# Optimization experiments

Measured on AMD Instinct MI355X. Metric: run time of the kernel, lower is better.

## Reference

```python
import jax, jax.numpy as jnp
import numpy as np

B, DIM, H, W = 8, 512, 32, 32
NUM_HEADS, KEY_DIM, VALUE_DIM, DIM_OUT = 8, 64, 64, 512


def setup_inputs() -> dict:
    key = jax.random.key(0)
    ks = jax.random.split(key, 5)
    return {
        "x": jax.random.normal(ks[0], (B, DIM, H, W), dtype=jnp.float32),
        "query_proj": jax.random.normal(ks[1], (NUM_HEADS, KEY_DIM, DIM), dtype=jnp.float32),
        "key_proj": jax.random.normal(ks[2], (DIM, KEY_DIM), dtype=jnp.float32),
        "value_proj": jax.random.normal(ks[3], (DIM, VALUE_DIM), dtype=jnp.float32),
        "out_proj": jax.random.normal(ks[4], (DIM_OUT, NUM_HEADS, VALUE_DIM), dtype=jnp.float32),
    }


def reference(x, query_proj, key_proj, value_proj, out_proj):
    b, d, h, w = x.shape
    key_dim = query_proj.shape[1]
    scale = key_dim ** (-0.5)
    # flatten spatial dims to tokens: [b, n, d] where n = h*w (m == x here)
    rx = jnp.transpose(x.reshape(b, d, h * w), (0, 2, 1))
    q = jnp.einsum('bnd,hkd->bnhk', rx, query_proj)
    k = jnp.einsum('bmd,dk->bmk', rx, key_proj)          # single shared K head
    attn = jax.nn.softmax(jnp.einsum('bnhk,bmk->bnhm', q, k) * scale, axis=-1)
    v = jnp.einsum('bmd,dv->bmv', rx, value_proj)        # single shared V head
    o = jnp.einsum('bnhm,bmv->bnhv', attn, v)
    result = jnp.einsum('bnhv,dhv->bdn', o, out_proj)
    return result.reshape(b, -1, h, w)
```

## Files before the change

### kernel.cpp

```cpp
#include <hip/hip_runtime.h>
#include <math.h>

#define BATCH 8
#define DIMD  512
#define NTOK  1024
#define NH    8
#define CQKV  640
#define DOUT  512

typedef __attribute__((ext_vector_type(8))) short short8;
typedef __attribute__((ext_vector_type(4))) short short4v;
typedef __attribute__((ext_vector_type(4))) float f32x4;

__device__ __forceinline__ short bf16rn(float x) {
    unsigned u = __float_as_uint(x);
    u += 0x7FFF + ((u >> 16) & 1);
    return (short)(u >> 16);
}
__device__ __forceinline__ float bf16tof(short s) {
    return __uint_as_float(((unsigned)(unsigned short)s) << 16);
}
struct HL { short h, l; };
__device__ __forceinline__ HL bf16split(float x) {
    HL r;
    r.h = bf16rn(x);
    r.l = bf16rn(x - bf16tof(r.h));
    return r;
}
__device__ __forceinline__ void dma16(const short* g, short* l) {
    __builtin_amdgcn_global_load_lds(
        (const __attribute__((address_space(1))) unsigned int*)g,
        (__attribute__((address_space(3))) unsigned int*)l, 16, 0, 0);
}
__device__ __forceinline__ float swzmax16(float v) {
    v = fmaxf(v, __int_as_float(__builtin_amdgcn_ds_swizzle(__float_as_int(v), 0x041F)));
    v = fmaxf(v, __int_as_float(__builtin_amdgcn_ds_swizzle(__float_as_int(v), 0x081F)));
    v = fmaxf(v, __int_as_float(__builtin_amdgcn_ds_swizzle(__float_as_int(v), 0x101F)));
    v = fmaxf(v, __int_as_float(__builtin_amdgcn_ds_swizzle(__float_as_int(v), 0x201F)));
    return v;
}
__device__ __forceinline__ unsigned packbf2(float f0, float f1) {
    return __builtin_amdgcn_perm(__float_as_uint(f1), __float_as_uint(f0), 0x07060302);
}


__global__ __launch_bounds__(256) void prepack_all(const float* __restrict__ x,
                                                   const float* __restrict__ qp,
                                                   const float* __restrict__ kp,
                                                   const float* __restrict__ vp,
                                                   const float* __restrict__ wout,
                                                   short* __restrict__ whi,
                                                   short* __restrict__ wlo,
                                                   short* __restrict__ xhi,
                                                   short* __restrict__ xlo,
                                                   short* __restrict__ wof) {
    __shared__ float Cs[64][65];
    const int blk = blockIdx.x;
    const int t = threadIdx.x;
    if (blk < 1024) {
        const int nt = blk & 15, dt = (blk >> 4) & 7, b = blk >> 7;
        #pragma unroll
        for (int i = 0; i < 4; ++i) {
            int row = (t >> 4) + i * 16;
            float4 v = *(const float4*)(x + ((size_t)(b * DIMD + dt * 64 + row)) * NTOK
                                          + nt * 64 + (t & 15) * 4);
            Cs[row][(t & 15) * 4 + 0] = v.x;
            Cs[row][(t & 15) * 4 + 1] = v.y;
            Cs[row][(t & 15) * 4 + 2] = v.z;
            Cs[row][(t & 15) * 4 + 3] = v.w;
        }
        __syncthreads();
        for (int u = t; u < 512; u += 256) {
            int lane2 = u & 63, cidx = u >> 6;
            int q2 = lane2 >> 4, r2 = lane2 & 15;
            int kt_loc = cidx & 1, mt_loc = cidx >> 1;
            short8 h8, l8;
            #pragma unroll
            for (int j = 0; j < 8; ++j) {
                HL s = bf16split(Cs[kt_loc * 32 + q2 * 8 + j][mt_loc * 16 + r2]);
                h8[j] = s.h; l8[j] = s.l;
            }
            size_t off = (((size_t)(b * 64 + nt * 4 + mt_loc)) * 16 + dt * 2 + kt_loc) * 512
                         + lane2 * 8;
            *(short8*)&xhi[off] = h8;
            *(short8*)&xlo[off] = l8;
        }
    } else if (blk < 1184) {
        int tid = (blk - 1024) * 256 + t;
        int lane = tid & 63, kt = (tid >> 6) & 15, ct = tid >> 10;
        int q = lane >> 4, r = lane & 15;
        int c = ct * 16 + r;
        short8 h, l;
        #pragma unroll
        for (int j = 0; j < 8; ++j) {
            int d = kt * 32 + q * 8 + j;
            float v;
            if (c < 64)       v = kp[d * 64 + c];
            else if (c < 128) v = vp[d * 64 + (c - 64)];
            else              v = qp[(size_t)(c - 128) * DIMD + d];
            HL s = bf16split(v);
            h[j] = s.h; l[j] = s.l;
        }
        *(short8*)&whi[(size_t)tid * 8] = h;
        *(short8*)&wlo[(size_t)tid * 8] = l;
    } else {
        int tid = (blk - 1184) * 256 + t;
        int lane = tid & 63, kt = (tid >> 6) & 15, mt = tid >> 10;
        int q = lane >> 4, r = lane & 15;
        const float* src = wout + (size_t)(mt * 16 + r) * DOUT + kt * 32 + q * 8;
        short8 h;
        #pragma unroll
        for (int j = 0; j < 8; ++j) h[j] = bf16rn(src[j]);
        *(short8*)&wof[(size_t)tid * 8] = h;
    }
}

__global__ __launch_bounds__(256) void qkv_gemm(const short* __restrict__ xhi,
                                                const short* __restrict__ xlo,
                                                const short* __restrict__ whi,
                                                const short* __restrict__ wlo,
                                                short* __restrict__ khi,
                                                short* __restrict__ klo,
                                                short* __restrict__ vf,
                                                short* __restrict__ qhi,
                                                short* __restrict__ qlo) {
    __shared__ __align__(16) char pool[32768];
    short* Ah = (short*)pool;
    short* Al = Ah + 4096;
    short* Bh = Al + 4096;
    short* Bl = Bh + 4096;
    float (*Cs)[65] = (float(*)[65])pool;

    const int b = blockIdx.z, bm = blockIdx.y, cb = blockIdx.x;
    const int tid = threadIdx.x, w = tid >> 6, lane = tid & 63;
    const int q = lane >> 4, r = lane & 15;
    f32x4 acc[4];
    #pragma unroll
    for (int j = 0; j < 4; ++j) acc[j] = (f32x4){0.f, 0.f, 0.f, 0.f};

    for (int it = 0; it < 8; ++it) {
        __syncthreads();
        for (int u = w; u < 8; u += 4) {
            size_t ga = ((size_t)((b * 64 + bm * 4 + (u >> 1)) * 16 + it * 2 + (u & 1))) * 512 + lane * 8;
            dma16(xhi + ga, &Ah[u * 512]);
            dma16(xlo + ga, &Al[u * 512]);
            size_t gb = ((size_t)((cb * 4 + (u >> 1)) * 16 + it * 2 + (u & 1))) * 512 + lane * 8;
            dma16(whi + gb, &Bh[u * 512]);
            dma16(wlo + gb, &Bl[u * 512]);
        }
        __syncthreads();
        #pragma unroll
        for (int kc = 0; kc < 2; ++kc) {
            short8 ah = *(short8*)&Ah[(w * 2 + kc) * 512 + lane * 8];
            short8 al = *(short8*)&Al[(w * 2 + kc) * 512 + lane * 8];
            #pragma unroll
            for (int tt = 0; tt < 4; ++tt) {
                short8 bh = *(short8*)&Bh[(tt * 2 + kc) * 512 + lane * 8];
                short8 bl = *(short8*)&Bl[(tt * 2 + kc) * 512 + lane * 8];
                acc[tt] = __builtin_amdgcn_mfma_f32_16x16x32_bf16(ah, bh, acc[tt], 0, 0, 0);
                acc[tt] = __builtin_amdgcn_mfma_f32_16x16x32_bf16(ah, bl, acc[tt], 0, 0, 0);
                acc[tt] = __builtin_amdgcn_mfma_f32_16x16x32_bf16(al, bh, acc[tt], 0, 0, 0);
            }
        }
    }

    __syncthreads();
    #pragma unroll
    for (int reg = 0; reg < 4; ++reg)
        #pragma unroll
        for (int tt = 0; tt < 4; ++tt)
            Cs[w * 16 + q * 4 + reg][tt * 16 + r] = acc[tt][reg];
    __syncthreads();

    if (cb == 0) {
        for (int u = tid; u < 512; u += 256) {
            int lane2 = u & 63, ic = u >> 6;
            int q2 = lane2 >> 4, r2 = lane2 & 15;
            int i = ic >> 1, cc = ic & 1;
            short8 h8, l8;
            #pragma unroll
            for (int j = 0; j < 8; ++j) {
                HL s = bf16split(Cs[i * 16 + r2][cc * 32 + q2 * 8 + j]);
                h8[j] = s.h; l8[j] = s.l;
            }
            size_t off = ((size_t)(b * 16 + bm) * 8 + ic) * 512 + lane2 * 8;
            *(short8*)&khi[off] = h8;
            *(short8*)&klo[off] = l8;
        }
    } else if (cb == 1) {
        for (int u = tid; u < 512; u += 256) {
            int lane2 = u & 63, ic = u >> 6;
            int q2 = lane2 >> 4, r2 = lane2 & 15;
            int tv = ic >> 1, cc = ic & 1;
            short8 v8;
            #pragma unroll
            for (int j = 0; j < 8; ++j)
                v8[j] = bf16rn(Cs[cc * 32 + q2 * 8 + j][tv * 16 + r2]);
            size_t off = ((size_t)(b * 16 + bm) * 8 + ic) * 512 + lane2 * 8;
            *(short8*)&vf[off] = v8;
        }
    } else {
        const int hd = cb - 2;
        const float qscale = 0.125f * 1.44269504f;
        for (int u = tid; u < 512; u += 256) {
            int lane2 = u & 63, ic = u >> 6;
            int q2 = lane2 >> 4, r2 = lane2 & 15;
            int ntl = ic >> 1, kc = ic & 1;
            short8 h8, l8;
            #pragma unroll
            for (int j = 0; j < 8; ++j) {
                HL s = bf16split(Cs[ntl * 16 + r2][kc * 32 + q2 * 8 + j] * qscale);
                h8[j] = s.h; l8[j] = s.l;
            }
            size_t off = ((((size_t)(b * 8 + hd) * 64 + bm * 4 + ntl) * 2 + kc) * 64 + lane2) * 8;
            *(short8*)&qhi[off] = h8;
            *(short8*)&qlo[off] = l8;
        }
    }
}

__global__ __launch_bounds__(256) void attn_mfma(const short* __restrict__ qhi_g,
                                                 const short* __restrict__ qlo_g,
                                                 const short* __restrict__ khi_g,
                                                 const short* __restrict__ klo_g,
                                                 const short* __restrict__ vf_g,
                                                 short* __restrict__ ob) {
    __shared__ short Khi[4096], Klo[4096], Vf[4096];
    __shared__ short Pbuf[4 * 64 * 36];
    const int blk = blockIdx.x;
    const int b   = blk & 7;
    const int h   = (blk >> 3) & 7;
    const int qt  = blk >> 6;
    const int tid = threadIdx.x;
    const int w    = tid >> 6;
    const int lane = tid & 63;
    const int q    = lane >> 4;
    const int r    = lane & 15;
    short* Pw = Pbuf + w * (64 * 36);

    short8 qhi[2][2], qlo[2][2];
    #pragma unroll
    for (int rt = 0; rt < 2; ++rt) {
        const int nt = qt * 8 + w * 2 + rt;
        #pragma unroll
        for (int c = 0; c < 2; ++c) {
            size_t off = ((((size_t)(b * 8 + h) * 64 + nt) * 2 + c) * 64 + lane) * 8;
            qhi[rt][c] = *(const short8*)&qhi_g[off];
            qlo[rt][c] = *(const short8*)&qlo_g[off];
        }
    }

    short8 bones;
    #pragma unroll
    for (int j = 0; j < 8; ++j) bones[j] = (short)0x3F80;

    f32x4 oacc[2][4], lacc[2];
    float m_[2][4];
    #pragma unroll
    for (int rt = 0; rt < 2; ++rt) {
        #pragma unroll
        for (int tt = 0; tt < 4; ++tt) oacc[rt][tt] = (f32x4){0.f, 0.f, 0.f, 0.f};
        lacc[rt] = (f32x4){0.f, 0.f, 0.f, 0.f};
        #pragma unroll
        for (int i = 0; i < 4; ++i) m_[rt][i] = -1e30f;
    }

    for (int t = 0; t < 16; ++t) {
        __syncthreads();
        const size_t kb = ((size_t)(b * 16 + t) * 8) * 512;
        for (int ch = w; ch < 8; ch += 4) {
            dma16(khi_g + kb + ch * 512 + lane * 8, &Khi[ch * 512]);
            dma16(klo_g + kb + ch * 512 + lane * 8, &Klo[ch * 512]);
            dma16(vf_g  + kb + ch * 512 + lane * 8, &Vf [ch * 512]);
        }
        __syncthreads();

        f32x4 s[2][4];
        #pragma unroll
        for (int rt = 0; rt < 2; ++rt)
            #pragma unroll
            for (int tt = 0; tt < 4; ++tt) s[rt][tt] = (f32x4){0.f, 0.f, 0.f, 0.f};
        #pragma unroll
        for (int c = 0; c < 2; ++c) {
            #pragma unroll
            for (int tt = 0; tt < 4; ++tt) {
                short8 kh = *(short8*)&Khi[((tt * 2 + c) * 64 + lane) * 8];
                short8 kl = *(short8*)&Klo[((tt * 2 + c) * 64 + lane) * 8];
                #pragma unroll
                for (int rt = 0; rt < 2; ++rt) {
                    s[rt][tt] = __builtin_amdgcn_mfma_f32_16x16x32_bf16(qhi[rt][c], kh, s[rt][tt], 0, 0, 0);
                    s[rt][tt] = __builtin_amdgcn_mfma_f32_16x16x32_bf16(qhi[rt][c], kl, s[rt][tt], 0, 0, 0);
                    s[rt][tt] = __builtin_amdgcn_mfma_f32_16x16x32_bf16(qlo[rt][c], kh, s[rt][tt], 0, 0, 0);
                }
            }
        }

        #pragma unroll
        for (int rt = 0; rt < 2; ++rt) {
            #pragma unroll
            for (int reg = 0; reg < 4; ++reg) {
                float smax = fmaxf(fmaxf(s[rt][0][reg], s[rt][1][reg]),
                                   fmaxf(s[rt][2][reg], s[rt][3][reg]));
                smax = swzmax16(smax);
                float nm    = fmaxf(m_[rt][reg], smax);
                float alpha = exp2f(m_[rt][reg] - nm);
                m_[rt][reg] = nm;
                #pragma unroll
                for (int tt = 0; tt < 4; ++tt)
                    s[rt][tt][reg] = exp2f(s[rt][tt][reg] - nm);
                lacc[rt][reg] *= alpha;
                #pragma unroll
                for (int tt = 0; tt < 4; ++tt) oacc[rt][tt][reg] *= alpha;
            }
        }

        #pragma unroll
        for (int rt = 0; rt < 2; ++rt) {
            #pragma unroll
            for (int tt = 0; tt < 4; ++tt) {
                uint2 pk;
                pk.x = packbf2(s[rt][tt][0], s[rt][tt][1]);
                pk.y = packbf2(s[rt][tt][2], s[rt][tt][3]);
                *(uint2*)&Pw[(r + 16 * tt) * 36 + rt * 16 + q * 4] = pk;
            }
        }

        #pragma unroll
        for (int c = 0; c < 2; ++c) {
            short8 pf[2];
            #pragma unroll
            for (int rt = 0; rt < 2; ++rt)
                #pragma unroll
                for (int j = 0; j < 8; ++j)
                    pf[rt][j] = Pw[(c * 32 + q * 8 + j) * 36 + rt * 16 + r];
            #pragma unroll
            for (int rt = 0; rt < 2; ++rt)
                lacc[rt] = __builtin_amdgcn_mfma_f32_16x16x32_bf16(pf[rt], bones, lacc[rt], 0, 0, 0);
            #pragma unroll
            for (int tt = 0; tt < 4; ++tt) {
                short8 vfr = *(short8*)&Vf[((tt * 2 + c) * 64 + lane) * 8];
                #pragma unroll
                for (int rt = 0; rt < 2; ++rt)
                    oacc[rt][tt] = __builtin_amdgcn_mfma_f32_16x16x32_bf16(pf[rt], vfr, oacc[rt][tt], 0, 0, 0);
            }
        }
    }

    #pragma unroll
    for (int rt = 0; rt < 2; ++rt) {
        const int nt = qt * 8 + w * 2 + rt;
        #pragma unroll
        for (int reg = 0; reg < 4; ++reg) {
            float inv = 1.f / lacc[rt][reg];
            #pragma unroll
            for (int tt = 0; tt < 4; ++tt) {
                int ct = h * 2 + (tt >> 1);
                int lanep = ((tt & 1) * 2 + (r >> 3)) * 16 + q * 4 + reg;
                ob[((((size_t)b * 64 + nt) * 16 + ct) * 64 + lanep) * 8 + (r & 7)] =
                    bf16rn(oacc[rt][tt][reg] * inv);
            }
        }
    }
}

__global__ __launch_bounds__(256) void out_gemm(const short* __restrict__ wof,
                                                const short* __restrict__ obf,
                                                float* __restrict__ out) {
    __shared__ short Ah[2][4096];
    __shared__ short Bh[2][4096];
    const int b = blockIdx.z, bd = blockIdx.y, bn = blockIdx.x;
    const int tid = threadIdx.x, w = tid >> 6, lane = tid & 63;
    const int q = lane >> 4, r = lane & 15;
    f32x4 acc[4];
    #pragma unroll
    for (int j = 0; j < 4; ++j) acc[j] = (f32x4){0.f, 0.f, 0.f, 0.f};

    for (int u = w; u < 8; u += 4) {
        size_t ga = ((size_t)((bd * 4 + (u >> 1)) * 16 + (u & 1))) * 512 + lane * 8;
        dma16(wof + ga, &Ah[0][u * 512]);
        size_t gb = ((size_t)((b * 64 + bn * 4 + (u >> 1)) * 16 + (u & 1))) * 512 + lane * 8;
        dma16(obf + gb, &Bh[0][u * 512]);
    }

    for (int it = 0; it < 8; ++it) {
        const int cur = it & 1;
        __syncthreads();
        if (it < 7) {
            for (int u = w; u < 8; u += 4) {
                size_t ga = ((size_t)((bd * 4 + (u >> 1)) * 16 + (it + 1) * 2 + (u & 1))) * 512 + lane * 8;
                dma16(wof + ga, &Ah[cur ^ 1][u * 512]);
                size_t gb = ((size_t)((b * 64 + bn * 4 + (u >> 1)) * 16 + (it + 1) * 2 + (u & 1))) * 512 + lane * 8;
                dma16(obf + gb, &Bh[cur ^ 1][u * 512]);
            }
        }
        #pragma unroll
        for (int kc = 0; kc < 2; ++kc) {
            short8 a = *(short8*)&Ah[cur][(w * 2 + kc) * 512 + lane * 8];
            #pragma unroll
            for (int tt = 0; tt < 4; ++tt) {
                short8 bb = *(short8*)&Bh[cur][(tt * 2 + kc) * 512 + lane * 8];
                acc[tt] = __builtin_amdgcn_mfma_f32_16x16x32_bf16(a, bb, acc[tt], 0, 0, 0);
            }
        }
    }
    const int d_base = bd * 64 + w * 16;
    #pragma unroll
    for (int reg = 0; reg < 4; ++reg)
        #pragma unroll
        for (int tt = 0; tt < 4; ++tt)
            out[((size_t)b * DOUT + d_base + q * 4 + reg) * NTOK
                + bn * 64 + tt * 16 + r] = acc[tt][reg];
}

extern "C" void kernel_launch(void* const* d_in, const int* in_sizes, int n_in,
                              void* d_out, int out_size, void* d_ws, size_t ws_size,
                              hipStream_t stream) {
    const float* x  = (const float*)d_in[0];
    const float* qp = (const float*)d_in[1];
    const float* kp = (const float*)d_in[2];
    const float* vp = (const float*)d_in[3];
    const float* op = (const float*)d_in[4];
    float* out = (float*)d_out;

    short* Whi = (short*)d_ws;
    short* Wlo = Whi + 327680;
    short* Xhi = Wlo + 327680;
    short* Xlo = Xhi + 4194304;
    short* Qhi = Xlo + 4194304;
    short* Qlo = Qhi + 4194304;
    short* Khi = Qlo + 4194304;
    short* Klo = Khi + 524288;
    short* Vf  = Klo + 524288;
    short* Wof = Vf  + 524288;
    short* Ob  = Xhi;

    prepack_all <<<1312, 256, 0, stream>>>(x, qp, kp, vp, op,
                                           Whi, Wlo, Xhi, Xlo, Wof);
    qkv_gemm    <<<dim3(10, 16, BATCH), 256, 0, stream>>>(Xhi, Xlo, Whi, Wlo,
                                                          Khi, Klo, Vf, Qhi, Qlo);
    attn_mfma   <<<512, 256, 0, stream>>>(Qhi, Qlo, Khi, Klo, Vf, Ob);
    out_gemm    <<<dim3(16, 8, BATCH), 256, 0, stream>>>(Wof, Ob, out);
}
```

Baseline: 181.9 us.

## Add lazy softmax rescaling in attention and swizzle QKV GEMM block order

The attention kernel now checks whether any new per-row partial maximum exceeds the running max by more than a threshold (30 in log2 units). It performs the cross-lane max reduction and the rescaling of the accumulators only when a wave needs it, and otherwise exponentiates against the stale max. This removes swizzle reductions and alpha multiplies from most iterations, at the cost of relying on the bf16/fp32 range to tolerate values up to 2^30 before renormalisation. Separately, the QKV GEMM is launched on a 1D grid with a remapped block index that groups 8 row tiles per column block, which should improve L2 reuse of the weight tiles.

```diff
diff --git a/kernel.cpp b/kernel.cpp
--- a/kernel.cpp
+++ b/kernel.cpp
@@ -131,7 +131,12 @@
     short* Bl = Bh + 4096;
     float (*Cs)[65] = (float(*)[65])pool;
 
-    const int b = blockIdx.z, bm = blockIdx.y, cb = blockIdx.x;
+    const int idx = blockIdx.x;
+    const int low = idx & 7, rest = idx >> 3;
+    const int cb = rest % 10, gh = rest / 10;
+    const int g = gh * 8 + low;
+    const int b = g >> 4, bm = g & 15;
+
     const int tid = threadIdx.x, w = tid >> 6, lane = tid & 63;
     const int q = lane >> 4, r = lane & 15;
     f32x4 acc[4];
@@ -295,24 +300,38 @@
             }
         }
 
-        #pragma unroll
-        for (int rt = 0; rt < 2; ++rt) {
+        float pmax[2][4];
+        bool need = false;
+        #pragma unroll
+        for (int rt = 0; rt < 2; ++rt)
             #pragma unroll
             for (int reg = 0; reg < 4; ++reg) {
-                float smax = fmaxf(fmaxf(s[rt][0][reg], s[rt][1][reg]),
-                                   fmaxf(s[rt][2][reg], s[rt][3][reg]));
-                smax = swzmax16(smax);
-                float nm    = fmaxf(m_[rt][reg], smax);
-                float alpha = exp2f(m_[rt][reg] - nm);
-                m_[rt][reg] = nm;
+                float pm = fmaxf(fmaxf(s[rt][0][reg], s[rt][1][reg]),
+                                 fmaxf(s[rt][2][reg], s[rt][3][reg]));
+                pmax[rt][reg] = pm;
+                need = need || (pm > m_[rt][reg] + 30.f);
+            }
+        if (__any((int)need)) {
+            #pragma unroll
+            for (int rt = 0; rt < 2; ++rt)
+                #pragma unroll
+                for (int reg = 0; reg < 4; ++reg) {
+                    float smax = swzmax16(pmax[rt][reg]);
+                    float nm    = fmaxf(m_[rt][reg], smax);
+                    float alpha = exp2f(m_[rt][reg] - nm);
+                    m_[rt][reg] = nm;
+                    lacc[rt][reg] *= alpha;
+                    #pragma unroll
+                    for (int tt = 0; tt < 4; ++tt) oacc[rt][tt][reg] *= alpha;
+                }
+        }
+        #pragma unroll
+        for (int rt = 0; rt < 2; ++rt)
+            #pragma unroll
+            for (int reg = 0; reg < 4; ++reg)
                 #pragma unroll
                 for (int tt = 0; tt < 4; ++tt)
-                    s[rt][tt][reg] = exp2f(s[rt][tt][reg] - nm);
-                lacc[rt][reg] *= alpha;
-                #pragma unroll
-                for (int tt = 0; tt < 4; ++tt) oacc[rt][tt][reg] *= alpha;
-            }
-        }
+                    s[rt][tt][reg] = exp2f(s[rt][tt][reg] - m_[rt][reg]);
 
         #pragma unroll
         for (int rt = 0; rt < 2; ++rt) {
@@ -436,8 +455,8 @@
 
     prepack_all <<<1312, 256, 0, stream>>>(x, qp, kp, vp, op,
                                            Whi, Wlo, Xhi, Xlo, Wof);
-    qkv_gemm    <<<dim3(10, 16, BATCH), 256, 0, stream>>>(Xhi, Xlo, Whi, Wlo,
-                                                          Khi, Klo, Vf, Qhi, Qlo);
+    qkv_gemm    <<<1280, 256, 0, stream>>>(Xhi, Xlo, Whi, Wlo,
+                                           Khi, Klo, Vf, Qhi, Qlo);
     attn_mfma   <<<512, 256, 0, stream>>>(Qhi, Qlo, Khi, Klo, Vf, Ob);
     out_gemm    <<<dim3(16, 8, BATCH), 256, 0, stream>>>(Wof, Ob, out);
 }
```

New measurement: 173.9 us. 1.05x faster.
